# Optimization experiments

Measured on AMD Instinct MI355X. Metric: run time of the kernel, lower is better.

## Reference

```python
import jax, jax.numpy as jnp
import numpy as np

NUM_FREQ = 32
MAX_POS = 10000.0
COORD_DIM = 3
EMB_DIM = COORD_DIM * NUM_FREQ * 2  # 192
KIN = 2 * EMB_DIM                   # 384
C = 32
T = 4
N_Y = 50000
N_X = 32768
K = 8
E = N_X * K
MLP_DIMS = [KIN, 128, 256, 128, C]


def sinusoidal_embed(p):
    # transformer-style sinusoidal embedding: [n, d] -> [n, d*NUM_FREQ*2]
    freqs = (1.0 / MAX_POS) ** (jnp.arange(NUM_FREQ, dtype=p.dtype) / NUM_FREQ)
    ang = p[..., None] * freqs                       # [n, d, nf]
    emb = jnp.stack([jnp.sin(ang), jnp.cos(ang)], axis=-1)  # [n, d, nf, 2]
    return emb.reshape(p.shape[0], -1)


def setup_inputs() -> dict:
    key = jax.random.key(0)
    ks = jax.random.split(key, 16)
    inp = {
        "y": jax.random.uniform(ks[0], (N_Y, COORD_DIM), dtype=jnp.float32),
        "x": jax.random.uniform(ks[1], (N_X, COORD_DIM), dtype=jnp.float32),
        "f_y": jax.random.normal(ks[2], (T, N_Y, C), dtype=jnp.float32),
        "neighbors_index": jax.random.randint(ks[3], (E,), 0, N_Y, dtype=jnp.int64),
    }
    # channel MLP params: 384 -> 128 -> 256 -> 128 -> 32, gelu between layers
    for i in range(4):
        fan_in, fan_out = MLP_DIMS[i], MLP_DIMS[i + 1]
        s = 1.0 / np.sqrt(fan_in)
        inp[f"W{i}"] = jax.random.uniform(ks[4 + 2 * i], (fan_in, fan_out), jnp.float32, -s, s)
        inp[f"b{i}"] = jax.random.uniform(ks[5 + 2 * i], (fan_out,), jnp.float32, -s, s)
    return inp


def reference(y, x, f_y, neighbors_index, W0, b0, W1, b1, W2, b2, W3, b3):
    n_x = x.shape[0]
    k = neighbors_index.shape[0] // n_x
    y_emb = sinusoidal_embed(y)            # [n_y, 192]
    x_emb = sinusoidal_embed(x)            # [n_x, 192]
    rep = y_emb[neighbors_index]           # [E, 192] gather per edge
    slf = jnp.repeat(x_emb, k, axis=0)     # [E, 192] query embedding per edge
    h = jnp.concatenate([rep, slf], axis=-1)  # [E, 384]
    h = jax.nn.gelu(h @ W0 + b0)
    h = jax.nn.gelu(h @ W1 + b1)
    h = jax.nn.gelu(h @ W2 + b2)
    kern = h @ W3 + b3                     # [E, C] kernel values
    in_feat = f_y[:, neighbors_index, :]   # [T, E, C] gathered source features
    prod = kern[None, :, :] * in_feat      # linear transform: k(x,y) * f(y)
    # reduction='sum' over each query's neighborhood (uniform K segments)
    out = prod.reshape(f_y.shape[0], n_x, k, -1).sum(axis=2)  # [T, n_x, C]
    return out
```

## Files before the change

### kernel.cpp

```cpp
#include <hip/hip_runtime.h>
#include <stdint.h>

#define EMB_DIM 192
#define CDIM 32
#define TDIM 4
#define N_Y 50000
#define N_X 32768
#define KNBR 8
#define ECNT (N_X*KNBR)

#define H1S 134
#define H2S 262
#define KS  33
#define ES  200

typedef __attribute__((ext_vector_type(8))) short bf16x8;
typedef __attribute__((ext_vector_type(4))) float f32x4;

static __device__ __forceinline__ short f2bf(float f){
  unsigned u = __float_as_uint(f);
  return (short)((u + 0x7FFFu) >> 16);
}
static __device__ __forceinline__ float geluf(float x){
  float x2 = x * x;
  float u  = __builtin_fmaf(0.044715f, x2, 1.0f);
  float p  = x * -1.5957691216057308f;
  float e  = __expf(p * u);
  return x * __builtin_amdgcn_rcpf(1.0f + e);
}

__global__ __launch_bounds__(256) void transpose_all(
    const float* __restrict__ W0, const float* __restrict__ W1,
    const float* __restrict__ W2, const float* __restrict__ W3,
    short* __restrict__ w0yt, short* __restrict__ w0xt,
    short* __restrict__ w1t, short* __restrict__ w2t, short* __restrict__ w3t){
  int id = blockIdx.x * 256 + threadIdx.x;
  if (id < 24576) {
    int n = id / 192, k = id - n * 192;
    w0yt[id] = f2bf(W0[k * 128 + n]);
  } else if (id < 49152) {
    int loc = id - 24576; int n = loc / 192, k = loc - n * 192;
    w0xt[loc] = f2bf(W0[(k + 192) * 128 + n]);
  } else if (id < 81920) {
    int loc = id - 49152; int n = loc / 128, k = loc - n * 128;
    w1t[loc] = f2bf(W1[k * 256 + n]);
  } else if (id < 114688) {
    int loc = id - 81920; int n = loc / 256, k = loc - n * 256;
    w2t[loc] = f2bf(W2[k * 128 + n]);
  } else if (id < 118784) {
    int loc = id - 114688; int n = loc / 128, k = loc - n * 128;
    w3t[loc] = f2bf(W3[k * 32 + n]);
  }
}

__global__ __launch_bounds__(256, 2) void precompute_c(
    const float* __restrict__ ypts, const float* __restrict__ xpts,
    const short* __restrict__ w0yt, const short* __restrict__ w0xt,
    const float* __restrict__ b0,
    short* __restrict__ c_y, float* __restrict__ c_x)
{
  __shared__ __attribute__((aligned(16))) short s_e[64 * ES];
  const int tid = threadIdx.x;
  const bool isY = blockIdx.x < 782;
  const int row0 = isY ? blockIdx.x * 64 : (blockIdx.x - 782) * 64;
  const int wave = tid >> 6, lane = tid & 63;
  const int quad = lane >> 4, l15 = lane & 15;

  {
    const int r = tid >> 2, q = tid & 3;
    const int grow = row0 + r;
    const bool valid = isY ? (grow < N_Y) : true;
    const float* src = isY ? (ypts + (size_t)grow * 3) : (xpts + (size_t)grow * 3);
    float c[3] = {0.f, 0.f, 0.f};
    if (valid) { c[0] = src[0]; c[1] = src[1]; c[2] = src[2]; }
    #pragma unroll
    for (int j = 0; j < 24; ++j) {
      int p = q * 24 + j;
      int d = p >> 5, i = p & 31;
      float f = __expf(-0.28782313662425575f * (float)i);
      float s, co;
      __sincosf(c[d] * f, &s, &co);
      unsigned u0 = __float_as_uint(s), u1 = __float_as_uint(co);
      unsigned pk = ((u0 + 0x7FFFu) >> 16) | (((u1 + 0x7FFFu) >> 16) << 16);
      *(unsigned*)&s_e[r * ES + d * 64 + 2 * i] = pk;
    }
  }
  __syncthreads();

  const short* w0t = isY ? w0yt : w0xt;
  f32x4 acc[4][2];
  #pragma unroll
  for (int mt = 0; mt < 4; ++mt)
    #pragma unroll
    for (int nt = 0; nt < 2; ++nt) acc[mt][nt] = (f32x4){0.f, 0.f, 0.f, 0.f};
  #pragma unroll
  for (int ch = 0; ch < 6; ++ch) {
    bf16x8 a[4], b[2];
    #pragma unroll
    for (int mt = 0; mt < 4; ++mt)
      a[mt] = *(const bf16x8*)&s_e[(mt * 16 + l15) * ES + ch * 32 + quad * 8];
    #pragma unroll
    for (int nt = 0; nt < 2; ++nt)
      b[nt] = *(const bf16x8*)&w0t[(size_t)(wave * 32 + nt * 16 + l15) * 192 + ch * 32 + quad * 8];
    #pragma unroll
    for (int mt = 0; mt < 4; ++mt)
      #pragma unroll
      for (int nt = 0; nt < 2; ++nt)
        acc[mt][nt] = __builtin_amdgcn_mfma_f32_16x16x32_bf16(a[mt], b[nt], acc[mt][nt], 0, 0, 0);
  }
  #pragma unroll
  for (int nt = 0; nt < 2; ++nt) {
    int col = wave * 32 + nt * 16 + l15;
    float bias = isY ? 0.f : b0[col];
    #pragma unroll
    for (int mt = 0; mt < 4; ++mt)
      #pragma unroll
      for (int rg = 0; rg < 4; ++rg) {
        int grow = row0 + mt * 16 + quad * 4 + rg;
        if (isY) { if (grow < N_Y) c_y[(size_t)grow * 128 + col] = f2bf(acc[mt][nt][rg]); }
        else     { c_x[(size_t)grow * 128 + col] = acc[mt][nt][rg] + bias; }
      }
  }
}

__global__ __launch_bounds__(256, 3) void fused_edge(
    const short* __restrict__ c_y, const float* __restrict__ c_x,
    const int* __restrict__ nidx, const float* __restrict__ f_y,
    const short* __restrict__ w1t, const float* __restrict__ b1,
    const short* __restrict__ w2t, const float* __restrict__ b2,
    const short* __restrict__ w3t, const float* __restrict__ b3,
    float* __restrict__ out)
{
  __shared__ __attribute__((aligned(16))) char smem[50688];
  short* s_h2   = (short*)smem;
  float* s_kern = (float*)smem;
  short* s_h1   = (short*)(smem + 33536);

  const int tid  = threadIdx.x;
  const int e0   = blockIdx.x * 64;
  const int wave = tid >> 6, lane = tid & 63;
  const int quad = lane >> 4, l15 = lane & 15;

  {
    const int r = tid >> 2, q = tid & 3;
    const int idx = nidx[e0 + r];
    const uint4*  cyp = (const uint4*)(c_y + (size_t)idx * 128 + q * 32);
    const float4* cxp = (const float4*)(c_x + (size_t)((e0 + r) >> 3) * 128 + q * 32);
    uint4  cyv[4];
    float4 cxv[8];
    #pragma unroll
    for (int i = 0; i < 4; ++i) cyv[i] = cyp[i];
    #pragma unroll
    for (int i = 0; i < 8; ++i) cxv[i] = cxp[i];
    const float* cxa = (const float*)cxv;
    const unsigned* cya = (const unsigned*)cyv;
    unsigned* dst = (unsigned*)&s_h1[r * H1S + q * 32];
    #pragma unroll
    for (int jj = 0; jj < 16; ++jj) {
      unsigned u = cya[jj];
      float lo = __uint_as_float(u << 16)         + cxa[2 * jj];
      float hi = __uint_as_float(u & 0xffff0000u) + cxa[2 * jj + 1];
      unsigned pk = (unsigned)(unsigned short)f2bf(geluf(lo)) |
                    ((unsigned)(unsigned short)f2bf(geluf(hi)) << 16);
      dst[jj] = pk;
    }
  }
  __syncthreads();

  {
    f32x4 acc1[4][4];
    #pragma unroll
    for (int mt = 0; mt < 4; ++mt)
      #pragma unroll
      for (int nt = 0; nt < 4; ++nt) acc1[mt][nt] = (f32x4){0.f, 0.f, 0.f, 0.f};
    #pragma unroll
    for (int ch = 0; ch < 4; ++ch) {
      bf16x8 a[4], b[4];
      #pragma unroll
      for (int mt = 0; mt < 4; ++mt)
        a[mt] = *(const bf16x8*)&s_h1[(mt * 16 + l15) * H1S + ch * 32 + quad * 8];
      #pragma unroll
      for (int nt = 0; nt < 4; ++nt)
        b[nt] = *(const bf16x8*)&w1t[(size_t)(wave * 64 + nt * 16 + l15) * 128 + ch * 32 + quad * 8];
      #pragma unroll
      for (int mt = 0; mt < 4; ++mt)
        #pragma unroll
        for (int nt = 0; nt < 4; ++nt)
          acc1[mt][nt] = __builtin_amdgcn_mfma_f32_16x16x32_bf16(a[mt], b[nt], acc1[mt][nt], 0, 0, 0);
    }
    #pragma unroll
    for (int nt = 0; nt < 4; ++nt) {
      int col = wave * 64 + nt * 16 + l15;
      float bias = b1[col];
      #pragma unroll
      for (int mt = 0; mt < 4; ++mt)
        #pragma unroll
        for (int rg = 0; rg < 4; ++rg) {
          int row = mt * 16 + quad * 4 + rg;
          s_h2[row * H2S + col] = f2bf(geluf(acc1[mt][nt][rg] + bias));
        }
    }
  }
  __syncthreads();

  {
    f32x4 acc2[4][2];
    #pragma unroll
    for (int mt = 0; mt < 4; ++mt)
      #pragma unroll
      for (int nt = 0; nt < 2; ++nt) acc2[mt][nt] = (f32x4){0.f, 0.f, 0.f, 0.f};
    #pragma unroll
    for (int ch = 0; ch < 8; ++ch) {
      bf16x8 a[4], b[2];
      #pragma unroll
      for (int mt = 0; mt < 4; ++mt)
        a[mt] = *(const bf16x8*)&s_h2[(mt * 16 + l15) * H2S + ch * 32 + quad * 8];
      #pragma unroll
      for (int nt = 0; nt < 2; ++nt)
        b[nt] = *(const bf16x8*)&w2t[(size_t)(wave * 32 + nt * 16 + l15) * 256 + ch * 32 + quad * 8];
      #pragma unroll
      for (int mt = 0; mt < 4; ++mt)
        #pragma unroll
        for (int nt = 0; nt < 2; ++nt)
          acc2[mt][nt] = __builtin_amdgcn_mfma_f32_16x16x32_bf16(a[mt], b[nt], acc2[mt][nt], 0, 0, 0);
    }
    #pragma unroll
    for (int nt = 0; nt < 2; ++nt) {
      int col = wave * 32 + nt * 16 + l15;
      float bias = b2[col];
      #pragma unroll
      for (int mt = 0; mt < 4; ++mt)
        #pragma unroll
        for (int rg = 0; rg < 4; ++rg) {
          int row = mt * 16 + quad * 4 + rg;
          s_h1[row * H1S + col] = f2bf(geluf(acc2[mt][nt][rg] + bias));
        }
    }
  }
  __syncthreads();

  {
    f32x4 acc3[2];
    acc3[0] = (f32x4){0.f, 0.f, 0.f, 0.f};
    acc3[1] = (f32x4){0.f, 0.f, 0.f, 0.f};
    #pragma unroll
    for (int ch = 0; ch < 4; ++ch) {
      bf16x8 a3 = *(const bf16x8*)&s_h1[(wave * 16 + l15) * H1S + ch * 32 + quad * 8];
      #pragma unroll
      for (int nt = 0; nt < 2; ++nt) {
        bf16x8 b3f = *(const bf16x8*)&w3t[(size_t)(nt * 16 + l15) * 128 + ch * 32 + quad * 8];
        acc3[nt] = __builtin_amdgcn_mfma_f32_16x16x32_bf16(a3, b3f, acc3[nt], 0, 0, 0);
      }
    }
    #pragma unroll
    for (int nt = 0; nt < 2; ++nt) {
      int col = nt * 16 + l15;
      float bias = b3[col];
      #pragma unroll
      for (int rg = 0; rg < 4; ++rg) {
        int row = wave * 16 + quad * 4 + rg;
        s_kern[row * KS + col] = acc3[nt][rg] + bias;
      }
    }
  }
  __syncthreads();

  {
    const int xloc = tid >> 5;
    const int c    = tid & 31;
    float acc[TDIM] = {0.f, 0.f, 0.f, 0.f};
    const int ebase = xloc * 8;
    #pragma unroll
    for (int j = 0; j < KNBR; ++j) {
      float kv = s_kern[(ebase + j) * KS + c];
      int idx = nidx[e0 + ebase + j];
      const float* fp = f_y + (size_t)idx * CDIM + c;
      #pragma unroll
      for (int t = 0; t < TDIM; ++t)
        acc[t] += kv * fp[(size_t)t * N_Y * CDIM];
    }
    const int xg = blockIdx.x * 8 + xloc;
    #pragma unroll
    for (int t = 0; t < TDIM; ++t)
      out[((size_t)t * N_X + xg) * CDIM + c] = acc[t];
  }
}

extern "C" void kernel_launch(void* const* d_in, const int* in_sizes, int n_in,
                              void* d_out, int out_size, void* d_ws, size_t ws_size,
                              hipStream_t stream)
{
  const float* y   = (const float*)d_in[0];
  const float* x   = (const float*)d_in[1];
  const float* f_y = (const float*)d_in[2];
  const int*  nidx = (const int*)d_in[3];
  const float* W0 = (const float*)d_in[4];  const float* b0 = (const float*)d_in[5];
  const float* W1 = (const float*)d_in[6];  const float* b1 = (const float*)d_in[7];
  const float* W2 = (const float*)d_in[8];  const float* b2 = (const float*)d_in[9];
  const float* W3 = (const float*)d_in[10]; const float* b3 = (const float*)d_in[11];

  char* ws = (char*)d_ws;
  short* c_y  = (short*)(ws + 0);
  float* c_x  = (float*)(ws + 12800000);
  short* w0yt = (short*)(ws + 29577216);
  short* w0xt = (short*)(ws + 29626368);
  short* w1t  = (short*)(ws + 29675520);
  short* w2t  = (short*)(ws + 29741056);
  short* w3t  = (short*)(ws + 29806592);

  hipLaunchKernelGGL(transpose_all, dim3((118784 + 255) / 256), dim3(256), 0, stream,
                     W0, W1, W2, W3, w0yt, w0xt, w1t, w2t, w3t);
  hipLaunchKernelGGL(precompute_c, dim3(782 + 512), dim3(256), 0, stream,
                     y, x, w0yt, w0xt, b0, c_y, c_x);
  hipLaunchKernelGGL(fused_edge, dim3(ECNT / 64), dim3(256), 0, stream,
                     c_y, c_x, nidx, f_y, w1t, b1, w2t, b2, w3t, b3, (float*)d_out);
}
```

Measured before the change: 241.9 us.

## Split layer-1/layer-2 MLP into halves to shrink LDS and raise occupancy

The 256-wide hidden layer of the edge MLP is now computed in two 128-column halves. Each half is staged in a 128-wide LDS buffer and immediately accumulated into the layer-2 accumulators. This cuts shared memory from about 50 KB to 34 KB per block and raises the launch-bounds minimum to 4 blocks per CU, trading extra barriers for occupancy. It also uses the hardware packed bf16 convert when available and writes the first layer's activations to LDS as 16-byte stores.

```diff
diff --git a/kernel.cpp b/kernel.cpp
--- a/kernel.cpp
+++ b/kernel.cpp
@@ -10,7 +10,6 @@
 #define ECNT (N_X*KNBR)
 
 #define H1S 134
-#define H2S 262
 #define KS  33
 #define ES  200
 
@@ -20,6 +19,21 @@
 static __device__ __forceinline__ short f2bf(float f){
   unsigned u = __float_as_uint(f);
   return (short)((u + 0x7FFFu) >> 16);
+}
+static __device__ __forceinline__ unsigned pk_bf16(float lo, float hi){
+#if defined(__has_builtin)
+#if __has_builtin(__builtin_amdgcn_cvt_pk_bf16_f32)
+  typedef __attribute__((ext_vector_type(2))) __bf16 bf16x2_t;
+  bf16x2_t v = __builtin_amdgcn_cvt_pk_bf16_f32(lo, hi);
+  return *(unsigned*)&v;
+#else
+  return ((__float_as_uint(lo) + 0x7FFFu) >> 16) |
+         ((((__float_as_uint(hi) + 0x7FFFu) >> 16)) << 16);
+#endif
+#else
+  return ((__float_as_uint(lo) + 0x7FFFu) >> 16) |
+         ((((__float_as_uint(hi) + 0x7FFFu) >> 16)) << 16);
+#endif
 }
 static __device__ __forceinline__ float geluf(float x){
   float x2 = x * x;
@@ -80,9 +94,7 @@
       float f = __expf(-0.28782313662425575f * (float)i);
       float s, co;
       __sincosf(c[d] * f, &s, &co);
-      unsigned u0 = __float_as_uint(s), u1 = __float_as_uint(co);
-      unsigned pk = ((u0 + 0x7FFFu) >> 16) | (((u1 + 0x7FFFu) >> 16) << 16);
-      *(unsigned*)&s_e[r * ES + d * 64 + 2 * i] = pk;
+      *(unsigned*)&s_e[r * ES + d * 64 + 2 * i] = pk_bf16(s, co);
     }
   }
   __syncthreads();
@@ -123,7 +135,7 @@
   }
 }
 
-__global__ __launch_bounds__(256, 3) void fused_edge(
+__global__ __launch_bounds__(256, 4) void fused_edge(
     const short* __restrict__ c_y, const float* __restrict__ c_x,
     const int* __restrict__ nidx, const float* __restrict__ f_y,
     const short* __restrict__ w1t, const float* __restrict__ b1,
@@ -131,10 +143,10 @@
     const short* __restrict__ w3t, const float* __restrict__ b3,
     float* __restrict__ out)
 {
-  __shared__ __attribute__((aligned(16))) char smem[50688];
-  short* s_h2   = (short*)smem;
+  __shared__ __attribute__((aligned(16))) char smem[34304];
+  short* s_hh   = (short*)smem;
   float* s_kern = (float*)smem;
-  short* s_h1   = (short*)(smem + 33536);
+  short* s_h1   = (short*)(smem + 17152);
 
   const int tid  = threadIdx.x;
   const int e0   = blockIdx.x * 64;
@@ -154,88 +166,96 @@
     for (int i = 0; i < 8; ++i) cxv[i] = cxp[i];
     const float* cxa = (const float*)cxv;
     const unsigned* cya = (const unsigned*)cyv;
-    unsigned* dst = (unsigned*)&s_h1[r * H1S + q * 32];
+    unsigned pk[16];
     #pragma unroll
     for (int jj = 0; jj < 16; ++jj) {
       unsigned u = cya[jj];
       float lo = __uint_as_float(u << 16)         + cxa[2 * jj];
       float hi = __uint_as_float(u & 0xffff0000u) + cxa[2 * jj + 1];
-      unsigned pk = (unsigned)(unsigned short)f2bf(geluf(lo)) |
-                    ((unsigned)(unsigned short)f2bf(geluf(hi)) << 16);
-      dst[jj] = pk;
-    }
+      pk[jj] = pk_bf16(geluf(lo), geluf(hi));
+    }
+    uint4* dst = (uint4*)&s_h1[r * H1S + q * 32];
+    #pragma unroll
+    for (int jj = 0; jj < 4; ++jj)
+      dst[jj] = *(uint4*)&pk[jj * 4];
   }
   __syncthreads();
 
-  {
-    f32x4 acc1[4][4];
-    #pragma unroll
-    for (int mt = 0; mt < 4; ++mt)
-      #pragma unroll
-      for (int nt = 0; nt < 4; ++nt) acc1[mt][nt] = (f32x4){0.f, 0.f, 0.f, 0.f};
+  f32x4 acc2[4][2];
+  #pragma unroll
+  for (int mt = 0; mt < 4; ++mt)
+    #pragma unroll
+    for (int nt = 0; nt < 2; ++nt) acc2[mt][nt] = (f32x4){0.f, 0.f, 0.f, 0.f};
+
+  #pragma unroll
+  for (int half = 0; half < 2; ++half) {
+    {
+      f32x4 acc1[4][2];
+      #pragma unroll
+      for (int mt = 0; mt < 4; ++mt)
+        #pragma unroll
+        for (int nt = 0; nt < 2; ++nt) acc1[mt][nt] = (f32x4){0.f, 0.f, 0.f, 0.f};
+      #pragma unroll
+      for (int ch = 0; ch < 4; ++ch) {
+        bf16x8 a[4], b[2];
+        #pragma unroll
+        for (int mt = 0; mt < 4; ++mt)
+          a[mt] = *(const bf16x8*)&s_h1[(mt * 16 + l15) * H1S + ch * 32 + quad * 8];
+        #pragma unroll
+        for (int nt = 0; nt < 2; ++nt)
+          b[nt] = *(const bf16x8*)&w1t[(size_t)(half * 128 + wave * 32 + nt * 16 + l15) * 128
+                                       + ch * 32 + quad * 8];
+        #pragma unroll
+        for (int mt = 0; mt < 4; ++mt)
+          #pragma unroll
+          for (int nt = 0; nt < 2; ++nt)
+            acc1[mt][nt] = __builtin_amdgcn_mfma_f32_16x16x32_bf16(a[mt], b[nt], acc1[mt][nt], 0, 0, 0);
+      }
+      #pragma unroll
+      for (int nt = 0; nt < 2; ++nt) {
+        int lcol = wave * 32 + nt * 16 + l15;
+        float bias = b1[half * 128 + lcol];
+        #pragma unroll
+        for (int mt = 0; mt < 4; ++mt)
+          #pragma unroll
+          for (int rg = 0; rg < 4; ++rg) {
+            int row = mt * 16 + quad * 4 + rg;
+            s_hh[row * H1S + lcol] = f2bf(geluf(acc1[mt][nt][rg] + bias));
+          }
+      }
+    }
+    __syncthreads();
+
     #pragma unroll
     for (int ch = 0; ch < 4; ++ch) {
-      bf16x8 a[4], b[4];
+      bf16x8 a[4], b[2];
       #pragma unroll
       for (int mt = 0; mt < 4; ++mt)
-        a[mt] = *(const bf16x8*)&s_h1[(mt * 16 + l15) * H1S + ch * 32 + quad * 8];
-      #pragma unroll
-      for (int nt = 0; nt < 4; ++nt)
-        b[nt] = *(const bf16x8*)&w1t[(size_t)(wave * 64 + nt * 16 + l15) * 128 + ch * 32 + quad * 8];
-      #pragma unroll
-      for (int mt = 0; mt < 4; ++mt)
-        #pragma unroll
-        for (int nt = 0; nt < 4; ++nt)
-          acc1[mt][nt] = __builtin_amdgcn_mfma_f32_16x16x32_bf16(a[mt], b[nt], acc1[mt][nt], 0, 0, 0);
-    }
-    #pragma unroll
-    for (int nt = 0; nt < 4; ++nt) {
-      int col = wave * 64 + nt * 16 + l15;
-      float bias = b1[col];
-      #pragma unroll
-      for (int mt = 0; mt < 4; ++mt)
-        #pragma unroll
-        for (int rg = 0; rg < 4; ++rg) {
-          int row = mt * 16 + quad * 4 + rg;
-          s_h2[row * H2S + col] = f2bf(geluf(acc1[mt][nt][rg] + bias));
-        }
-    }
-  }
-  __syncthreads();
-
-  {
-    f32x4 acc2[4][2];
-    #pragma unroll
-    for (int mt = 0; mt < 4; ++mt)
-      #pragma unroll
-      for (int nt = 0; nt < 2; ++nt) acc2[mt][nt] = (f32x4){0.f, 0.f, 0.f, 0.f};
-    #pragma unroll
-    for (int ch = 0; ch < 8; ++ch) {
-      bf16x8 a[4], b[2];
-      #pragma unroll
-      for (int mt = 0; mt < 4; ++mt)
-        a[mt] = *(const bf16x8*)&s_h2[(mt * 16 + l15) * H2S + ch * 32 + quad * 8];
+        a[mt] = *(const bf16x8*)&s_hh[(mt * 16 + l15) * H1S + ch * 32 + quad * 8];
       #pragma unroll
       for (int nt = 0; nt < 2; ++nt)
-        b[nt] = *(const bf16x8*)&w2t[(size_t)(wave * 32 + nt * 16 + l15) * 256 + ch * 32 + quad * 8];
+        b[nt] = *(const bf16x8*)&w2t[(size_t)(wave * 32 + nt * 16 + l15) * 256
+                                     + half * 128 + ch * 32 + quad * 8];
       #pragma unroll
       for (int mt = 0; mt < 4; ++mt)
         #pragma unroll
         for (int nt = 0; nt < 2; ++nt)
           acc2[mt][nt] = __builtin_amdgcn_mfma_f32_16x16x32_bf16(a[mt], b[nt], acc2[mt][nt], 0, 0, 0);
     }
-    #pragma unroll
-    for (int nt = 0; nt < 2; ++nt) {
-      int col = wave * 32 + nt * 16 + l15;
-      float bias = b2[col];
-      #pragma unroll
-      for (int mt = 0; mt < 4; ++mt)
-        #pragma unroll
-        for (int rg = 0; rg < 4; ++rg) {
-          int row = mt * 16 + quad * 4 + rg;
-          s_h1[row * H1S + col] = f2bf(geluf(acc2[mt][nt][rg] + bias));
-        }
-    }
+    __syncthreads();
+  }
+
+  #pragma unroll
+  for (int nt = 0; nt < 2; ++nt) {
+    int col = wave * 32 + nt * 16 + l15;
+    float bias = b2[col];
+    #pragma unroll
+    for (int mt = 0; mt < 4; ++mt)
+      #pragma unroll
+      for (int rg = 0; rg < 4; ++rg) {
+        int row = mt * 16 + quad * 4 + rg;
+        s_h1[row * H1S + col] = f2bf(geluf(acc2[mt][nt][rg] + bias));
+      }
   }
   __syncthreads();
 
```

After: 260.5 us. +7.7%, slower.

## Make fused_edge persistent with cross-tile gather prefetch and early f_y loads

Applied to the files above, without the earlier changes.

Converts fused_edge into a persistent kernel with 768 blocks that loop over the 4096 edge tiles. The next tile's c_y gather and the index for the tile after it are prefetched into registers so the random-gather latency overlaps with the MLP work. The f_y neighbor feature loads are issued during layer 2 instead of after the last barrier. It also adds packed bf16 conversion, vectorized LDS stores, and a barrier that waits only on LDS counters. The cost is higher register pressure from the 32-float prefetch buffer and the prefetched c_y, which may reduce occupancy. The persistent grid may also not fill the GPU evenly.

```diff
diff --git a/kernel.cpp b/kernel.cpp
--- a/kernel.cpp
+++ b/kernel.cpp
@@ -8,6 +8,8 @@
 #define N_X 32768
 #define KNBR 8
 #define ECNT (N_X*KNBR)
+#define NTILE 4096
+#define NBLK 768
 
 #define H1S 134
 #define H2S 262
@@ -20,6 +22,21 @@
 static __device__ __forceinline__ short f2bf(float f){
   unsigned u = __float_as_uint(f);
   return (short)((u + 0x7FFFu) >> 16);
+}
+static __device__ __forceinline__ unsigned pk_bf16(float lo, float hi){
+#if defined(__has_builtin)
+#if __has_builtin(__builtin_amdgcn_cvt_pk_bf16_f32)
+  typedef __attribute__((ext_vector_type(2))) __bf16 bf16x2_t;
+  bf16x2_t v = __builtin_amdgcn_cvt_pk_bf16_f32(lo, hi);
+  return *(unsigned*)&v;
+#else
+  return ((__float_as_uint(lo) + 0x7FFFu) >> 16) |
+         ((((__float_as_uint(hi) + 0x7FFFu) >> 16)) << 16);
+#endif
+#else
+  return ((__float_as_uint(lo) + 0x7FFFu) >> 16) |
+         ((((__float_as_uint(hi) + 0x7FFFu) >> 16)) << 16);
+#endif
 }
 static __device__ __forceinline__ float geluf(float x){
   float x2 = x * x;
@@ -27,6 +44,9 @@
   float p  = x * -1.5957691216057308f;
   float e  = __expf(p * u);
   return x * __builtin_amdgcn_rcpf(1.0f + e);
+}
+static __device__ __forceinline__ void barrier_lds(){
+  asm volatile("s_waitcnt lgkmcnt(0)\n\ts_barrier" ::: "memory");
 }
 
 __global__ __launch_bounds__(256) void transpose_all(
@@ -80,9 +100,7 @@
       float f = __expf(-0.28782313662425575f * (float)i);
       float s, co;
       __sincosf(c[d] * f, &s, &co);
-      unsigned u0 = __float_as_uint(s), u1 = __float_as_uint(co);
-      unsigned pk = ((u0 + 0x7FFFu) >> 16) | (((u1 + 0x7FFFu) >> 16) << 16);
-      *(unsigned*)&s_e[r * ES + d * 64 + 2 * i] = pk;
+      *(unsigned*)&s_e[r * ES + d * 64 + 2 * i] = pk_bf16(s, co);
     }
   }
   __syncthreads();
@@ -137,152 +155,180 @@
   short* s_h1   = (short*)(smem + 33536);
 
   const int tid  = threadIdx.x;
-  const int e0   = blockIdx.x * 64;
   const int wave = tid >> 6, lane = tid & 63;
   const int quad = lane >> 4, l15 = lane & 15;
-
+  const int r    = tid >> 2, q = tid & 3;
+  const int xloc = tid >> 5, cc = tid & 31;
+
+  int   pf_idx1;
+  uint4 pf_cy[4];
   {
-    const int r = tid >> 2, q = tid & 3;
-    const int idx = nidx[e0 + r];
-    const uint4*  cyp = (const uint4*)(c_y + (size_t)idx * 128 + q * 32);
-    const float4* cxp = (const float4*)(c_x + (size_t)((e0 + r) >> 3) * 128 + q * 32);
-    uint4  cyv[4];
-    float4 cxv[8];
-    #pragma unroll
-    for (int i = 0; i < 4; ++i) cyv[i] = cyp[i];
-    #pragma unroll
-    for (int i = 0; i < 8; ++i) cxv[i] = cxp[i];
-    const float* cxa = (const float*)cxv;
-    const unsigned* cya = (const unsigned*)cyv;
-    unsigned* dst = (unsigned*)&s_h1[r * H1S + q * 32];
-    #pragma unroll
-    for (int jj = 0; jj < 16; ++jj) {
-      unsigned u = cya[jj];
-      float lo = __uint_as_float(u << 16)         + cxa[2 * jj];
-      float hi = __uint_as_float(u & 0xffff0000u) + cxa[2 * jj + 1];
-      unsigned pk = (unsigned)(unsigned short)f2bf(geluf(lo)) |
-                    ((unsigned)(unsigned short)f2bf(geluf(hi)) << 16);
-      dst[jj] = pk;
-    }
-  }
-  __syncthreads();
-
-  {
-    f32x4 acc1[4][4];
-    #pragma unroll
-    for (int mt = 0; mt < 4; ++mt)
-      #pragma unroll
-      for (int nt = 0; nt < 4; ++nt) acc1[mt][nt] = (f32x4){0.f, 0.f, 0.f, 0.f};
-    #pragma unroll
-    for (int ch = 0; ch < 4; ++ch) {
-      bf16x8 a[4], b[4];
+    int idx0 = nidx[blockIdx.x * 64 + r];
+    const uint4* cyp = (const uint4*)(c_y + (size_t)idx0 * 128 + q * 32);
+    #pragma unroll
+    for (int i = 0; i < 4; ++i) pf_cy[i] = cyp[i];
+    int t1 = blockIdx.x + NBLK; if (t1 >= NTILE) t1 = blockIdx.x;
+    pf_idx1 = nidx[t1 * 64 + r];
+  }
+
+  for (int tile = blockIdx.x; tile < NTILE; tile += NBLK) {
+    const int e0 = tile * 64;
+
+    {
+      float4 cxv[8];
+      const float4* cxp = (const float4*)(c_x + (size_t)((e0 + r) >> 3) * 128 + q * 32);
+      #pragma unroll
+      for (int i = 0; i < 8; ++i) cxv[i] = cxp[i];
+      const float* cxa = (const float*)cxv;
+      const unsigned* cya = (const unsigned*)pf_cy;
+      unsigned pk[16];
+      #pragma unroll
+      for (int jj = 0; jj < 16; ++jj) {
+        unsigned u = cya[jj];
+        float lo = __uint_as_float(u << 16)         + cxa[2 * jj];
+        float hi = __uint_as_float(u & 0xffff0000u) + cxa[2 * jj + 1];
+        pk[jj] = pk_bf16(geluf(lo), geluf(hi));
+      }
+      uint4* dst = (uint4*)&s_h1[r * H1S + q * 32];
+      #pragma unroll
+      for (int jj = 0; jj < 4; ++jj)
+        dst[jj] = *(uint4*)&pk[jj * 4];
+    }
+
+    {
+      const uint4* cyp = (const uint4*)(c_y + (size_t)pf_idx1 * 128 + q * 32);
+      #pragma unroll
+      for (int i = 0; i < 4; ++i) pf_cy[i] = cyp[i];
+      int t2 = tile + 2 * NBLK; if (t2 >= NTILE) t2 = tile;
+      pf_idx1 = nidx[t2 * 64 + r];
+    }
+
+    barrier_lds();
+
+    {
+      f32x4 acc1[4][4];
       #pragma unroll
       for (int mt = 0; mt < 4; ++mt)
-        a[mt] = *(const bf16x8*)&s_h1[(mt * 16 + l15) * H1S + ch * 32 + quad * 8];
-      #pragma unroll
-      for (int nt = 0; nt < 4; ++nt)
-        b[nt] = *(const bf16x8*)&w1t[(size_t)(wave * 64 + nt * 16 + l15) * 128 + ch * 32 + quad * 8];
+        #pragma unroll
+        for (int nt = 0; nt < 4; ++nt) acc1[mt][nt] = (f32x4){0.f, 0.f, 0.f, 0.f};
+      #pragma unroll
+      for (int ch = 0; ch < 4; ++ch) {
+        bf16x8 a[4], b[4];
+        #pragma unroll
+        for (int mt = 0; mt < 4; ++mt)
+          a[mt] = *(const bf16x8*)&s_h1[(mt * 16 + l15) * H1S + ch * 32 + quad * 8];
+        #pragma unroll
+        for (int nt = 0; nt < 4; ++nt)
+          b[nt] = *(const bf16x8*)&w1t[(size_t)(wave * 64 + nt * 16 + l15) * 128 + ch * 32 + quad * 8];
+        #pragma unroll
+        for (int mt = 0; mt < 4; ++mt)
+          #pragma unroll
+          for (int nt = 0; nt < 4; ++nt)
+            acc1[mt][nt] = __builtin_amdgcn_mfma_f32_16x16x32_bf16(a[mt], b[nt], acc1[mt][nt], 0, 0, 0);
+      }
+      #pragma unroll
+      for (int nt = 0; nt < 4; ++nt) {
+        int col = wave * 64 + nt * 16 + l15;
+        float bias = b1[col];
+        #pragma unroll
+        for (int mt = 0; mt < 4; ++mt)
+          #pragma unroll
+          for (int rg = 0; rg < 4; ++rg) {
+            int row = mt * 16 + quad * 4 + rg;
+            s_h2[row * H2S + col] = f2bf(geluf(acc1[mt][nt][rg] + bias));
+          }
+      }
+    }
+    barrier_lds();
+
+    float fv[32];
+    {
+      f32x4 acc2[4][2];
       #pragma unroll
       for (int mt = 0; mt < 4; ++mt)
         #pragma unroll
-        for (int nt = 0; nt < 4; ++nt)
-          acc1[mt][nt] = __builtin_amdgcn_mfma_f32_16x16x32_bf16(a[mt], b[nt], acc1[mt][nt], 0, 0, 0);
-    }
-    #pragma unroll
-    for (int nt = 0; nt < 4; ++nt) {
-      int col = wave * 64 + nt * 16 + l15;
-      float bias = b1[col];
-      #pragma unroll
-      for (int mt = 0; mt < 4; ++mt)
+        for (int nt = 0; nt < 2; ++nt) acc2[mt][nt] = (f32x4){0.f, 0.f, 0.f, 0.f};
+      #pragma unroll
+      for (int ch = 0; ch < 8; ++ch) {
+        bf16x8 a[4], b[2];
+        #pragma unroll
+        for (int mt = 0; mt < 4; ++mt)
+          a[mt] = *(const bf16x8*)&s_h2[(mt * 16 + l15) * H2S + ch * 32 + quad * 8];
+        #pragma unroll
+        for (int nt = 0; nt < 2; ++nt)
+          b[nt] = *(const bf16x8*)&w2t[(size_t)(wave * 32 + nt * 16 + l15) * 256 + ch * 32 + quad * 8];
+        #pragma unroll
+        for (int mt = 0; mt < 4; ++mt)
+          #pragma unroll
+          for (int nt = 0; nt < 2; ++nt)
+            acc2[mt][nt] = __builtin_amdgcn_mfma_f32_16x16x32_bf16(a[mt], b[nt], acc2[mt][nt], 0, 0, 0);
+      }
+
+      #pragma unroll
+      for (int j = 0; j < KNBR; ++j) {
+        int idx = nidx[e0 + xloc * 8 + j];
+        const float* fp = f_y + (size_t)idx * CDIM + cc;
+        #pragma unroll
+        for (int t = 0; t < TDIM; ++t)
+          fv[j * 4 + t] = fp[(size_t)t * N_Y * CDIM];
+      }
+
+      #pragma unroll
+      for (int nt = 0; nt < 2; ++nt) {
+        int col = wave * 32 + nt * 16 + l15;
+        float bias = b2[col];
+        #pragma unroll
+        for (int mt = 0; mt < 4; ++mt)
+          #pragma unroll
+          for (int rg = 0; rg < 4; ++rg) {
+            int row = mt * 16 + quad * 4 + rg;
+            s_h1[row * H1S + col] = f2bf(geluf(acc2[mt][nt][rg] + bias));
+          }
+      }
+    }
+    barrier_lds();
+
+    {
+      f32x4 acc3[2];
+      acc3[0] = (f32x4){0.f, 0.f, 0.f, 0.f};
+      acc3[1] = (f32x4){0.f, 0.f, 0.f, 0.f};
+      #pragma unroll
+      for (int ch = 0; ch < 4; ++ch) {
+        bf16x8 a3 = *(const bf16x8*)&s_h1[(wave * 16 + l15) * H1S + ch * 32 + quad * 8];
+        #pragma unroll
+        for (int nt = 0; nt < 2; ++nt) {
+          bf16x8 b3f = *(const bf16x8*)&w3t[(size_t)(nt * 16 + l15) * 128 + ch * 32 + quad * 8];
+          acc3[nt] = __builtin_amdgcn_mfma_f32_16x16x32_bf16(a3, b3f, acc3[nt], 0, 0, 0);
+        }
+      }
+      #pragma unroll
+      for (int nt = 0; nt < 2; ++nt) {
+        int col = nt * 16 + l15;
+        float bias = b3[col];
         #pragma unroll
         for (int rg = 0; rg < 4; ++rg) {
-          int row = mt * 16 + quad * 4 + rg;
-          s_h2[row * H2S + col] = f2bf(geluf(acc1[mt][nt][rg] + bias));
+          int row = wave * 16 + quad * 4 + rg;
+          s_kern[row * KS + col] = acc3[nt][rg] + bias;
         }
-    }
-  }
-  __syncthreads();
-
-  {
-    f32x4 acc2[4][2];
-    #pragma unroll
-    for (int mt = 0; mt < 4; ++mt)
-      #pragma unroll
-      for (int nt = 0; nt < 2; ++nt) acc2[mt][nt] = (f32x4){0.f, 0.f, 0.f, 0.f};
-    #pragma unroll
-    for (int ch = 0; ch < 8; ++ch) {
-      bf16x8 a[4], b[2];
-      #pragma unroll
-      for (int mt = 0; mt < 4; ++mt)
-        a[mt] = *(const bf16x8*)&s_h2[(mt * 16 + l15) * H2S + ch * 32 + quad * 8];
-      #pragma unroll
-      for (int nt = 0; nt < 2; ++nt)
-        b[nt] = *(const bf16x8*)&w2t[(size_t)(wave * 32 + nt * 16 + l15) * 256 + ch * 32 + quad * 8];
-      #pragma unroll
-      for (int mt = 0; mt < 4; ++mt)
-        #pragma unroll
-        for (int nt = 0; nt < 2; ++nt)
-          acc2[mt][nt] = __builtin_amdgcn_mfma_f32_16x16x32_bf16(a[mt], b[nt], acc2[mt][nt], 0, 0, 0);
-    }
-    #pragma unroll
-    for (int nt = 0; nt < 2; ++nt) {
-      int col = wave * 32 + nt * 16 + l15;
-      float bias = b2[col];
-      #pragma unroll
-      for (int mt = 0; mt < 4; ++mt)
-        #pragma unroll
-        for (int rg = 0; rg < 4; ++rg) {
-          int row = mt * 16 + quad * 4 + rg;
-          s_h1[row * H1S + col] = f2bf(geluf(acc2[mt][nt][rg] + bias));
-        }
-    }
-  }
-  __syncthreads();
-
-  {
-    f32x4 acc3[2];
-    acc3[0] = (f32x4){0.f, 0.f, 0.f, 0.f};
-    acc3[1] = (f32x4){0.f, 0.f, 0.f, 0.f};
-    #pragma unroll
-    for (int ch = 0; ch < 4; ++ch) {
-      bf16x8 a3 = *(const bf16x8*)&s_h1[(wave * 16 + l15) * H1S + ch * 32 + quad * 8];
-      #pragma unroll
-      for (int nt = 0; nt < 2; ++nt) {
-        bf16x8 b3f = *(const bf16x8*)&w3t[(size_t)(nt * 16 + l15) * 128 + ch * 32 + quad * 8];
-        acc3[nt] = __builtin_amdgcn_mfma_f32_16x16x32_bf16(a3, b3f, acc3[nt], 0, 0, 0);
-      }
-    }
-    #pragma unroll
-    for (int nt = 0; nt < 2; ++nt) {
-      int col = nt * 16 + l15;
-      float bias = b3[col];
-      #pragma unroll
-      for (int rg = 0; rg < 4; ++rg) {
-        int row = wave * 16 + quad * 4 + rg;
-        s_kern[row * KS + col] = acc3[nt][rg] + bias;
-      }
-    }
-  }
-  __syncthreads();
-
-  {
-    const int xloc = tid >> 5;
-    const int c    = tid & 31;
-    float acc[TDIM] = {0.f, 0.f, 0.f, 0.f};
-    const int ebase = xloc * 8;
-    #pragma unroll
-    for (int j = 0; j < KNBR; ++j) {
-      float kv = s_kern[(ebase + j) * KS + c];
-      int idx = nidx[e0 + ebase + j];
-      const float* fp = f_y + (size_t)idx * CDIM + c;
+      }
+    }
+    barrier_lds();
+
+    {
+      float acc[TDIM] = {0.f, 0.f, 0.f, 0.f};
+      const int ebase = xloc * 8;
+      #pragma unroll
+      for (int j = 0; j < KNBR; ++j) {
+        float kv = s_kern[(ebase + j) * KS + cc];
+        #pragma unroll
+        for (int t = 0; t < TDIM; ++t)
+          acc[t] += kv * fv[j * 4 + t];
+      }
+      const int xg = tile * 8 + xloc;
       #pragma unroll
       for (int t = 0; t < TDIM; ++t)
-        acc[t] += kv * fp[(size_t)t * N_Y * CDIM];
-    }
-    const int xg = blockIdx.x * 8 + xloc;
-    #pragma unroll
-    for (int t = 0; t < TDIM; ++t)
-      out[((size_t)t * N_X + xg) * CDIM + c] = acc[t];
+        out[((size_t)t * N_X + xg) * CDIM + cc] = acc[t];
+    }
   }
 }
 
@@ -312,6 +358,6 @@
                      W0, W1, W2, W3, w0yt, w0xt, w1t, w2t, w3t);
   hipLaunchKernelGGL(precompute_c, dim3(782 + 512), dim3(256), 0, stream,
                      y, x, w0yt, w0xt, b0, c_y, c_x);
-  hipLaunchKernelGGL(fused_edge, dim3(ECNT / 64), dim3(256), 0, stream,
+  hipLaunchKernelGGL(fused_edge, dim3(NBLK), dim3(256), 0, stream,
                      c_y, c_x, nidx, f_y, w1t, b1, w2t, b2, w3t, b3, (float*)d_out);
 }
```

New measurement: 276.2 us. 1.14x slower.
